# Optimization experiments

Measured on AMD Instinct MI355X. Metric: run time of the kernel, lower is better.

Reference implementation:

```python
import jax, jax.numpy as jnp
import numpy as np


def setup_inputs() -> dict:
    key = jax.random.key(0)
    ks = jax.random.split(key, 6)
    B, T, D, E, F = 2, 2048, 1024, 8, 2048
    x = jax.random.normal(ks[0], (B, T, D), dtype=jnp.float32)
    gate_w = jax.random.normal(ks[1], (D, E), dtype=jnp.float32) * (1.0 / np.sqrt(D))
    base_w1 = jax.random.normal(ks[2], (D, F), dtype=jnp.float32) * np.sqrt(2.0 / (D + F))
    base_w2 = jax.random.normal(ks[3], (F, D), dtype=jnp.float32) * np.sqrt(2.0 / (F + D))
    expert_w1 = base_w1[None] + jax.random.normal(ks[4], (E, D, F), dtype=jnp.float32) * 0.01
    expert_w2 = base_w2[None] + jax.random.normal(ks[5], (E, F, D), dtype=jnp.float32) * 0.01
    expert_b1 = jnp.zeros((E, F), dtype=jnp.float32)
    expert_b2 = jnp.zeros((E, D), dtype=jnp.float32)
    return {"x": x, "gate_w": gate_w, "expert_w1": expert_w1, "expert_b1": expert_b1,
            "expert_w2": expert_w2, "expert_b2": expert_b2}


def reference(x, gate_w, expert_w1, expert_b1, expert_w2, expert_b2):
    # Router (TopKRouter): top-2 routing with aux load-balance loss + z-loss
    E = gate_w.shape[-1]
    TOP_K = 2
    Z_LOSS_COEF = 1e-3
    logits = jnp.einsum('btd,de->bte', x, gate_w)                       # [B,T,E]
    top_vals, top_idx = jax.lax.top_k(logits, TOP_K)                    # [B,T,K]
    router_weights = jax.nn.softmax(top_vals, axis=-1)                  # [B,T,K]
    probs = jax.nn.softmax(logits, axis=-1)
    mask = jax.nn.one_hot(top_idx[..., 0], E, dtype=x.dtype)            # top-1 expert mask
    tokens_per_expert = mask.mean(axis=(0, 1))                          # [E]
    router_prob_per_expert = probs.mean(axis=(0, 1))                    # [E]
    aux_loss = E * jnp.sum(tokens_per_expert * router_prob_per_expert) \
               + jnp.mean(logits ** 2) * Z_LOSS_COEF

    # Expert FFNs: compute all experts densely, then gather top-k outputs.
    # (Same math as per-token weight gather, without the BTDF intermediate.)
    h = jnp.einsum('btd,edf->btef', x, expert_w1) + expert_b1           # [B,T,E,F]
    h = jax.nn.gelu(h, approximate=False)                               # torch F.gelu default = erf
    out_all = jnp.einsum('btef,efd->bted', h, expert_w2) + expert_b2    # [B,T,E,D]
    gathered = jnp.take_along_axis(out_all, top_idx[..., None], axis=2) # [B,T,K,D]
    output = jnp.einsum('btk,btkd->btd', router_weights, gathered)      # [B,T,D]
    return output, aux_loss
```

## Files before the change

### kernel.cpp

```cpp
#include <hip/hip_runtime.h>
#include <hip/hip_bf16.h>

#define NTOK 4096
#define DDIM 1024
#define NEXP 8
#define FDIM 2048
#define CAP  4096
#define RTOK 16

typedef float f32x4 __attribute__((ext_vector_type(4)));
typedef short s16x8 __attribute__((ext_vector_type(8)));
typedef short s16x4 __attribute__((ext_vector_type(4)));

__device__ __forceinline__ unsigned short f2bf(float f) {
  unsigned int u = __float_as_uint(f);
  unsigned int r = u + 0x7fffu + ((u >> 16) & 1u);
  return (unsigned short)(r >> 16);
}

__device__ __forceinline__ void gload16(const void* g, void* l) {
  __builtin_amdgcn_global_load_lds(
      (__attribute__((address_space(1))) unsigned int*)(g),
      (__attribute__((address_space(3))) unsigned int*)(l), 16, 0, 0);
}

__global__ void k_transpose_cast(const float* __restrict__ src, unsigned short* __restrict__ dst,
                                 int R, int C) {
  __shared__ float tile[32][33];
  int e = blockIdx.z;
  int c0 = blockIdx.x * 32, r0 = blockIdx.y * 32;
  const float* s = src + (size_t)e * R * C;
  unsigned short* d = dst + (size_t)e * R * C;
  int tx = threadIdx.x, ty = threadIdx.y;
  #pragma unroll
  for (int i = 0; i < 4; i++)
    tile[ty + i*8][tx] = s[(size_t)(r0 + ty + i*8) * C + (c0 + tx)];
  __syncthreads();
  #pragma unroll
  for (int i = 0; i < 4; i++)
    d[(size_t)(c0 + ty + i*8) * R + (r0 + tx)] = f2bf(tile[tx][ty + i*8]);
}

__global__ __launch_bounds__(128)
void k_router(const float* __restrict__ x, const float* __restrict__ gw,
              unsigned short* __restrict__ xb,
              float* __restrict__ topw, int* __restrict__ elist,
              int* __restrict__ ecnt, int* __restrict__ cnt1,
              float* __restrict__ psum, float* __restrict__ sqsum) {
  __shared__ float gwt[NEXP][DDIM + 4];
  __shared__ float xs[RTOK][264];
  __shared__ double lgd[RTOK][NEXP];
  __shared__ float bps[NEXP];
  __shared__ int bc[NEXP];
  __shared__ float bsq;
  const int tid = threadIdx.x;
  const int tok0 = blockIdx.x * RTOK;

  for (int i = tid; i < DDIM * NEXP; i += 128) {
    int d = i >> 3, e = i & 7;
    gwt[e][d] = gw[i];
  }
  if (tid < NEXP) { bps[tid] = 0.f; bc[tid] = 0; }
  if (tid == 0) bsq = 0.f;

  const int t = tid >> 3, e = tid & 7;
  double a0 = 0.0, a1 = 0.0, a2 = 0.0, a3 = 0.0;
  for (int c = 0; c < DDIM; c += 256) {
    __syncthreads();
    for (int i = tid; i < RTOK * 64; i += 128) {
      int r = i >> 6, c4 = i & 63;
      float4 v = *(const float4*)(x + (size_t)(tok0 + r) * DDIM + c + c4 * 4);
      *(float4*)&xs[r][c4 * 4] = v;
      s16x4 o;
      o[0] = (short)f2bf(v.x); o[1] = (short)f2bf(v.y);
      o[2] = (short)f2bf(v.z); o[3] = (short)f2bf(v.w);
      *(s16x4*)(xb + (size_t)(tok0 + r) * DDIM + c + c4 * 4) = o;
    }
    __syncthreads();
    #pragma unroll 8
    for (int d4 = 0; d4 < 64; d4++) {
      float4 xv = *(const float4*)&xs[t][d4 * 4];
      float4 gv = *(const float4*)&gwt[e][c + d4 * 4];
      a0 += (double)xv.x * (double)gv.x;
      a1 += (double)xv.y * (double)gv.y;
      a2 += (double)xv.z * (double)gv.z;
      a3 += (double)xv.w * (double)gv.w;
    }
  }
  lgd[t][e] = (a0 + a1) + (a2 + a3);
  __syncthreads();

  if (tid < RTOK) {
    int tok = tok0 + tid;
    double acc[NEXP];
    #pragma unroll
    for (int k = 0; k < NEXP; k++) acc[k] = lgd[tid][k];
    int i0 = 0; double v0 = acc[0];
    #pragma unroll
    for (int k = 1; k < NEXP; k++) if (acc[k] > v0) { v0 = acc[k]; i0 = k; }
    int i1 = (i0 == 0) ? 1 : 0; double v1 = acc[i1];
    #pragma unroll
    for (int k = 0; k < NEXP; k++) if (k != i0 && acc[k] > v1) { v1 = acc[k]; i1 = k; }
    float w0 = 1.0f / (1.0f + expf((float)(v1 - v0)));
    topw[2*tok] = w0; topw[2*tok + 1] = 1.0f - w0;
    int s0 = atomicAdd(&ecnt[i0], 1); elist[i0*CAP + s0] = 2*tok;
    int s1 = atomicAdd(&ecnt[i1], 1); elist[i1*CAP + s1] = 2*tok + 1;
    atomicAdd(&bc[i0], 1);
    float lm = (float)acc[0];
    #pragma unroll
    for (int k = 1; k < NEXP; k++) lm = fmaxf(lm, (float)acc[k]);
    float pe[NEXP], ps = 0.f, sq = 0.f;
    #pragma unroll
    for (int k = 0; k < NEXP; k++) {
      float le = (float)acc[k];
      pe[k] = expf(le - lm); ps += pe[k];
      sq += le * le;
    }
    float inv = 1.0f / ps;
    #pragma unroll
    for (int k = 0; k < NEXP; k++) atomicAdd(&bps[k], pe[k] * inv);
    atomicAdd(&bsq, sq);
  }
  __syncthreads();
  if (tid < NEXP) { atomicAdd(&psum[tid], bps[tid]); atomicAdd(&cnt1[tid], bc[tid]); }
  if (tid == 0) atomicAdd(sqsum, bsq);
}

template<int K, int N, bool GELU, bool ROWSHIFT>
__global__ __launch_bounds__(512)
void k_gemm(const unsigned short* __restrict__ A, const unsigned short* __restrict__ Bt,
            const float* __restrict__ bias, void* __restrict__ Out,
            const int* __restrict__ elist, const int* __restrict__ ecnt) {
  constexpr int BM = 128, BN = 128, BK = 128, WM = 2, WN = 4;
  constexpr int AISS = BM / 32;
  constexpr int BISS = BN / 32;
  constexpr int MF = BM / WM / 16;
  constexpr int NF = BN / WN / 16;
  __shared__ unsigned char lsA[BM * 256];
  __shared__ unsigned char lsB[BN * 256];
  const int e = blockIdx.z, mt = blockIdx.y, nt = blockIdx.x;
  const int cnt = ecnt[e];
  const int m0 = mt * BM;
  if (m0 >= cnt) return;
  const int rv = min(BM, cnt - m0);
  const int* lst = elist + e * CAP + m0;
  const int tid = threadIdx.x, wv = tid >> 6, lane = tid & 63;
  const int wm = wv / WN, wn = wv % WN;
  const unsigned short* Be = Bt + (size_t)e * N * K;

  const unsigned short* agp[AISS];
  const unsigned short* bgp[BISS];
  int adst[AISS], bdst[BISS];
  const int cu = tid & 15;
  #pragma unroll
  for (int li = 0; li < AISS; li++) {
    int r = li * 32 + (tid >> 4);
    int rr = (r < rv) ? r : 0;
    int aid = lst[rr];
    int arow = ROWSHIFT ? (aid >> 1) : aid;
    int csrc = (cu ^ (r & 15)) * 16;
    agp[li] = A + (size_t)arow * K + (csrc >> 1);
    adst[li] = r * 256 + cu * 16;
  }
  #pragma unroll
  for (int li = 0; li < BISS; li++) {
    int r = li * 32 + (tid >> 4);
    int csrc = (cu ^ (r & 15)) * 16;
    bgp[li] = Be + (size_t)(nt * BN + r) * K + (csrc >> 1);
    bdst[li] = r * 256 + cu * 16;
  }

  f32x4 acc[MF][NF];
  #pragma unroll
  for (int mi = 0; mi < MF; mi++)
    #pragma unroll
    for (int ni = 0; ni < NF; ni++)
      acc[mi][ni] = (f32x4){0.f, 0.f, 0.f, 0.f};

  constexpr int NK = K / BK;
  for (int t = 0; t < NK; ++t) {
    const int k0 = t * BK;
    #pragma unroll
    for (int li = 0; li < AISS; li++) gload16(agp[li] + k0, &lsA[adst[li]]);
    #pragma unroll
    for (int li = 0; li < BISS; li++) gload16(bgp[li] + k0, &lsB[bdst[li]]);
    __syncthreads();
    #pragma unroll
    for (int ks = 0; ks < 4; ks++) {
      s16x8 af[MF], bf[NF];
      #pragma unroll
      for (int mi = 0; mi < MF; mi++) {
        int row = wm * (BM / WM) + mi * 16 + (lane & 15);
        int c16 = (ks * 4 + (lane >> 4)) ^ (row & 15);
        af[mi] = *(const s16x8*)&lsA[row * 256 + c16 * 16];
      }
      #pragma unroll
      for (int ni = 0; ni < NF; ni++) {
        int row = wn * (BN / WN) + ni * 16 + (lane & 15);
        int c16 = (ks * 4 + (lane >> 4)) ^ (row & 15);
        bf[ni] = *(const s16x8*)&lsB[row * 256 + c16 * 16];
      }
      #pragma unroll
      for (int mi = 0; mi < MF; mi++)
        #pragma unroll
        for (int ni = 0; ni < NF; ni++)
          acc[mi][ni] = __builtin_amdgcn_mfma_f32_16x16x32_bf16(af[mi], bf[ni], acc[mi][ni], 0, 0, 0);
    }
    __syncthreads();
  }

  const int g4 = (lane >> 4) * 4, cn = lane & 15;
  #pragma unroll
  for (int mi = 0; mi < MF; mi++) {
    #pragma unroll
    for (int reg = 0; reg < 4; reg++) {
      int r = wm * (BM / WM) + mi * 16 + g4 + reg;
      if (r < rv) {
        int aid = lst[r];
        #pragma unroll
        for (int ni = 0; ni < NF; ni++) {
          int n = nt * BN + wn * (BN / WN) + ni * 16 + cn;
          float v = acc[mi][ni][reg] + bias[(size_t)e * N + n];
          if constexpr (GELU) {
            v = 0.5f * v * (1.0f + erff(v * 0.70710678118654752f));
            ((unsigned short*)Out)[(size_t)aid * N + n] = f2bf(v);
          } else {
            ((float*)Out)[(size_t)aid * N + n] = v;
          }
        }
      }
    }
  }
}

__global__ void k_combine(const float* __restrict__ buf, const float* __restrict__ topw,
                          float* __restrict__ out) {
  int i = blockIdx.x * 256 + threadIdx.x;
  int t = i >> 8, c = i & 255;
  float w0 = topw[2*t], w1 = topw[2*t + 1];
  float4 a = ((const float4*)(buf + (size_t)(2*t) * DDIM))[c];
  float4 b = ((const float4*)(buf + (size_t)(2*t + 1) * DDIM))[c];
  float4 o;
  o.x = w0*a.x + w1*b.x; o.y = w0*a.y + w1*b.y;
  o.z = w0*a.z + w1*b.z; o.w = w0*a.w + w1*b.w;
  ((float4*)out)[i] = o;
}

__global__ void k_aux(const int* __restrict__ cnt1, const float* __restrict__ psum,
                      const float* __restrict__ sqsum, float* __restrict__ out) {
  if (threadIdx.x == 0 && blockIdx.x == 0) {
    float a = 0.f;
    for (int e = 0; e < NEXP; e++)
      a += ((float)cnt1[e] / (float)NTOK) * (psum[e] / (float)NTOK);
    out[(size_t)NTOK * DDIM] = (float)NEXP * a + (*sqsum) / (float)(NTOK * NEXP) * 1e-3f;
  }
}

extern "C" void kernel_launch(void* const* d_in, const int* in_sizes, int n_in,
                              void* d_out, int out_size, void* d_ws, size_t ws_size,
                              hipStream_t stream) {
  const float* x  = (const float*)d_in[0];
  const float* gw = (const float*)d_in[1];
  const float* w1 = (const float*)d_in[2];
  const float* b1 = (const float*)d_in[3];
  const float* w2 = (const float*)d_in[4];
  const float* b2 = (const float*)d_in[5];
  float* out = (float*)d_out;
  char* p = (char*)d_ws;

  int*   ecnt  = (int*)p;
  int*   cnt1  = (int*)(p + 32);
  float* psum  = (float*)(p + 64);
  float* sqsum = (float*)(p + 96);
  float* topw  = (float*)(p + 256);
  int*   elist = (int*)(p + 256 + 32768);
  unsigned short* xb  = (unsigned short*)(p + 256 + 32768 + 131072);
  unsigned short* w1t = xb  + (size_t)NTOK * DDIM;
  unsigned short* w2t = w1t + (size_t)NEXP * DDIM * FDIM;
  unsigned short* Hb  = w2t + (size_t)NEXP * DDIM * FDIM;
  float* obuf = (float*)(Hb + (size_t)NTOK * 2 * FDIM);

  hipMemsetAsync(p, 0, 128, stream);
  k_transpose_cast<<<dim3(FDIM/32, DDIM/32, NEXP), dim3(32, 8), 0, stream>>>(w1, w1t, DDIM, FDIM);
  k_transpose_cast<<<dim3(DDIM/32, FDIM/32, NEXP), dim3(32, 8), 0, stream>>>(w2, w2t, FDIM, DDIM);
  k_router<<<NTOK / RTOK, 128, 0, stream>>>(x, gw, xb, topw, elist, ecnt, cnt1, psum, sqsum);
  k_gemm<DDIM, FDIM, true,  true ><<<dim3(FDIM/128, 16, NEXP), 512, 0, stream>>>(xb, w1t, b1, Hb, elist, ecnt);
  k_gemm<FDIM, DDIM, false, false><<<dim3(DDIM/128, 16, NEXP), 512, 0, stream>>>(Hb, w2t, b2, obuf, elist, ecnt);
  k_combine<<<NTOK * DDIM / 4 / 256, 256, 0, stream>>>(obuf, topw, out);
  k_aux<<<1, 64, 0, stream>>>(cnt1, psum, sqsum, out);
}
```

Baseline: 261.0 us.

## Fuse top-k combine into second GEMM epilogue via atomics; widen transpose tiles

The second expert GEMM now scales each row by its router weight and atomically adds it into the zeroed output, so the separate combine kernel and the fp32 intermediate buffer go away. The output is cleared with a memset before the work starts. The weight transpose-cast kernel now uses 64x64 tiles with float4 loads and 16-byte bf16 stores to cut memory transactions. The atomics cost scattered read-modify-write traffic, and float summation order becomes nondeterministic.

```diff
diff --git a/kernel.cpp b/kernel.cpp
--- a/kernel.cpp
+++ b/kernel.cpp
@@ -24,21 +24,34 @@
       (__attribute__((address_space(3))) unsigned int*)(l), 16, 0, 0);
 }
 
-__global__ void k_transpose_cast(const float* __restrict__ src, unsigned short* __restrict__ dst,
-                                 int R, int C) {
-  __shared__ float tile[32][33];
-  int e = blockIdx.z;
-  int c0 = blockIdx.x * 32, r0 = blockIdx.y * 32;
+__global__ __launch_bounds__(256)
+void k_transpose_cast(const float* __restrict__ src, unsigned short* __restrict__ dst,
+                      int R, int C) {
+  __shared__ float tile[64][68];
+  const int e = blockIdx.z;
+  const int c0 = blockIdx.x * 64, r0 = blockIdx.y * 64;
   const float* s = src + (size_t)e * R * C;
   unsigned short* d = dst + (size_t)e * R * C;
-  int tx = threadIdx.x, ty = threadIdx.y;
-  #pragma unroll
-  for (int i = 0; i < 4; i++)
-    tile[ty + i*8][tx] = s[(size_t)(r0 + ty + i*8) * C + (c0 + tx)];
+  const int tid = threadIdx.x;
+  const int lr = tid >> 4, lc = (tid & 15) * 4;
+  #pragma unroll
+  for (int p = 0; p < 4; p++) {
+    float4 v = *(const float4*)(s + (size_t)(r0 + p * 16 + lr) * C + c0 + lc);
+    tile[p * 16 + lr][lc]     = v.x;
+    tile[p * 16 + lr][lc + 1] = v.y;
+    tile[p * 16 + lr][lc + 2] = v.z;
+    tile[p * 16 + lr][lc + 3] = v.w;
+  }
   __syncthreads();
-  #pragma unroll
-  for (int i = 0; i < 4; i++)
-    d[(size_t)(c0 + ty + i*8) * R + (r0 + tx)] = f2bf(tile[tx][ty + i*8]);
+  const int sc = tid >> 3, sr = (tid & 7) * 8;
+  #pragma unroll
+  for (int p = 0; p < 2; p++) {
+    int c = p * 32 + sc;
+    s16x8 o;
+    #pragma unroll
+    for (int j = 0; j < 8; j++) o[j] = (short)f2bf(tile[sr + j][c]);
+    *(s16x8*)(d + (size_t)(c0 + c) * R + r0 + sr) = o;
+  }
 }
 
 __global__ __launch_bounds__(128)
@@ -130,7 +143,8 @@
 __global__ __launch_bounds__(512)
 void k_gemm(const unsigned short* __restrict__ A, const unsigned short* __restrict__ Bt,
             const float* __restrict__ bias, void* __restrict__ Out,
-            const int* __restrict__ elist, const int* __restrict__ ecnt) {
+            const int* __restrict__ elist, const int* __restrict__ ecnt,
+            const float* __restrict__ topw) {
   constexpr int BM = 128, BN = 128, BK = 128, WM = 2, WN = 4;
   constexpr int AISS = BM / 32;
   constexpr int BISS = BN / 32;
@@ -225,25 +239,12 @@
             v = 0.5f * v * (1.0f + erff(v * 0.70710678118654752f));
             ((unsigned short*)Out)[(size_t)aid * N + n] = f2bf(v);
           } else {
-            ((float*)Out)[(size_t)aid * N + n] = v;
+            atomicAdd(&((float*)Out)[(size_t)(aid >> 1) * N + n], topw[aid] * v);
           }
         }
       }
     }
   }
-}
-
-__global__ void k_combine(const float* __restrict__ buf, const float* __restrict__ topw,
-                          float* __restrict__ out) {
-  int i = blockIdx.x * 256 + threadIdx.x;
-  int t = i >> 8, c = i & 255;
-  float w0 = topw[2*t], w1 = topw[2*t + 1];
-  float4 a = ((const float4*)(buf + (size_t)(2*t) * DDIM))[c];
-  float4 b = ((const float4*)(buf + (size_t)(2*t + 1) * DDIM))[c];
-  float4 o;
-  o.x = w0*a.x + w1*b.x; o.y = w0*a.y + w1*b.y;
-  o.z = w0*a.z + w1*b.z; o.w = w0*a.w + w1*b.w;
-  ((float4*)out)[i] = o;
 }
 
 __global__ void k_aux(const int* __restrict__ cnt1, const float* __restrict__ psum,
@@ -278,14 +279,13 @@
   unsigned short* w1t = xb  + (size_t)NTOK * DDIM;
   unsigned short* w2t = w1t + (size_t)NEXP * DDIM * FDIM;
   unsigned short* Hb  = w2t + (size_t)NEXP * DDIM * FDIM;
-  float* obuf = (float*)(Hb + (size_t)NTOK * 2 * FDIM);
 
   hipMemsetAsync(p, 0, 128, stream);
-  k_transpose_cast<<<dim3(FDIM/32, DDIM/32, NEXP), dim3(32, 8), 0, stream>>>(w1, w1t, DDIM, FDIM);
-  k_transpose_cast<<<dim3(DDIM/32, FDIM/32, NEXP), dim3(32, 8), 0, stream>>>(w2, w2t, FDIM, DDIM);
+  hipMemsetAsync(out, 0, (size_t)(NTOK * DDIM + 1) * 4, stream);
+  k_transpose_cast<<<dim3(FDIM/64, DDIM/64, NEXP), 256, 0, stream>>>(w1, w1t, DDIM, FDIM);
+  k_transpose_cast<<<dim3(DDIM/64, FDIM/64, NEXP), 256, 0, stream>>>(w2, w2t, FDIM, DDIM);
   k_router<<<NTOK / RTOK, 128, 0, stream>>>(x, gw, xb, topw, elist, ecnt, cnt1, psum, sqsum);
-  k_gemm<DDIM, FDIM, true,  true ><<<dim3(FDIM/128, 16, NEXP), 512, 0, stream>>>(xb, w1t, b1, Hb, elist, ecnt);
-  k_gemm<FDIM, DDIM, false, false><<<dim3(DDIM/128, 16, NEXP), 512, 0, stream>>>(Hb, w2t, b2, obuf, elist, ecnt);
-  k_combine<<<NTOK * DDIM / 4 / 256, 256, 0, stream>>>(obuf, topw, out);
+  k_gemm<DDIM, FDIM, true,  true ><<<dim3(FDIM/128, 16, NEXP), 512, 0, stream>>>(xb, w1t, b1, Hb, elist, ecnt, nullptr);
+  k_gemm<FDIM, DDIM, false, false><<<dim3(DDIM/128, 16, NEXP), 512, 0, stream>>>(Hb, w2t, b2, out, elist, ecnt, topw);
   k_aux<<<1, 64, 0, stream>>>(cnt1, psum, sqsum, out);
 }
```

Result: slower. 277.5 us (+6.3%).
